# Kernel tuning notes

Hardware: AMD Instinct MI355X
Metric: run time of the kernel (lower is better)

The kernel has to match this reference:

```python
import jax, jax.numpy as jnp
import numpy as np

VOCAB = 128000
D = 256
N_BUBBLES = 256
N_EQ_STEPS = 5
SEQ_LEN = 512
ETA = 0.1      # relaxation rate toward input
KAPPA = 0.05   # mean-field coupling between bubbles


def setup_inputs() -> dict:
    key = jax.random.key(0)
    k1, k2, k3 = jax.random.split(key, 3)
    embed = jax.random.normal(k1, (VOCAB, D), dtype=jnp.float32)
    bubbles = jax.random.normal(k2, (N_BUBBLES, D), dtype=jnp.float32)
    memory_decay_base = jnp.asarray(0.8, dtype=jnp.float32)
    novelty_sensitivity = jnp.asarray(1.0, dtype=jnp.float32)
    tokens = jax.random.randint(k3, (SEQ_LEN,), 0, VOCAB, dtype=jnp.int64)
    return {"embed": embed, "bubbles": bubbles,
            "memory_decay_base": memory_decay_base,
            "novelty_sensitivity": novelty_sensitivity,
            "tokens": tokens}


def _foam_forward(x, bubbles):
    """x: [d]. Equilibrate bubble states, build density matrix, eigen-spectrum."""
    s = bubbles  # [n_bubbles, d]
    for _ in range(N_EQ_STEPS):  # fixed small hyperparam loop
        s = s + ETA * (x[None, :] - s) + KAPPA * (s.mean(axis=0, keepdims=True) - s)
        s = s / (jnp.linalg.norm(s, axis=-1, keepdims=True) + 1e-10)
    rho = (s.T @ s) / s.shape[0]  # [d, d] PSD, trace ~ 1
    w = jnp.linalg.eigvalsh(rho)  # ascending eigenvalues [d]
    w = jnp.clip(w, 0.0)
    output_dist = w / (w.sum() + 1e-10)
    return s, output_dist


def reference(embed, bubbles, memory_decay_base, novelty_sensitivity, tokens):
    sens = jnp.abs(novelty_sensitivity)

    def step(memory, tok):
        x = embed[tok]                      # [d]
        mem_mean = memory.mean(axis=0)      # [d]
        mem_norm = jnp.linalg.norm(mem_mean) + 1e-10
        x_norm = jnp.linalg.norm(x) + 1e-10
        novelty = jnp.where(mem_norm > 1e-8,
                            1.0 - jnp.dot(x, mem_mean) / (x_norm * mem_norm),
                            1.0)
        decay = jax.nn.sigmoid(memory_decay_base - sens * novelty)
        x_with_memory = x + decay * mem_mean
        eq, output_dist = _foam_forward(x_with_memory, bubbles)
        memory = decay * memory + (1.0 - decay) * eq
        return memory, output_dist

    memory0 = jnp.zeros_like(bubbles)  # [n_bubbles, d]
    _, dists = jax.lax.scan(step, memory0, tokens)
    return dists  # [seq_len, d] per-step eigenvalue distributions of rho
```

## Files before the change

### kernel.cpp

```cpp
#include <hip/hip_runtime.h>
#include <hip/hip_fp16.h>
#include <math.h>

#define SEQ 512
#define ETA 0.1f
#define KAPPA 0.05f
#define AA 0.85f

typedef _Float16 f16x8 __attribute__((ext_vector_type(8)));
typedef float f32x4 __attribute__((ext_vector_type(4)));

#define WS_G    ((size_t)0)
#define WS_GD   ((size_t)65536)
#define WS_M0   ((size_t)65792)
#define WS_BX   ((size_t)66048)
#define WS_X2   ((size_t)197120)
#define WS_ZS   ((size_t)197632)
#define WS_YS   ((size_t)328704)
#define WS_GS   ((size_t)459776)
#define WS_HS   ((size_t)984064)
#define WS_ALS  ((size_t)986112)
#define WS_BETS ((size_t)1117184)
#define WS_CT   ((size_t)1772544)

__device__ __forceinline__ float wred_sum(float v) {
#pragma unroll
  for (int m = 1; m < 64; m <<= 1) v += __shfl_xor(v, m, 64);
  return v;
}
__device__ __forceinline__ float wred_min(float v) {
#pragma unroll
  for (int m = 1; m < 64; m <<= 1) v = fminf(v, __shfl_xor(v, m, 64));
  return v;
}
__device__ __forceinline__ float wred_max(float v) {
#pragma unroll
  for (int m = 1; m < 64; m <<= 1) v = fmaxf(v, __shfl_xor(v, m, 64));
  return v;
}
__device__ __forceinline__ float rfl(float x) {
  return __builtin_bit_cast(float, __builtin_amdgcn_readfirstlane(__builtin_bit_cast(int, x)));
}

__global__ void k0_gram(const float* __restrict__ B, float* __restrict__ ws) {
  float* G = ws + WS_G;
  float* Gd = ws + WS_GD;
  __shared__ float bi[256];
  const int i = blockIdx.x, j = threadIdx.x;
  bi[j] = B[(size_t)i * 256 + j];
  __syncthreads();
  float a0 = 0.f, a1 = 0.f, a2 = 0.f, a3 = 0.f;
#pragma unroll
  for (int c = 0; c < 256; c += 4) {
    float4 b4 = *(const float4*)&B[(size_t)j * 256 + c];
    a0 = fmaf(bi[c + 0], b4.x, a0);
    a1 = fmaf(bi[c + 1], b4.y, a1);
    a2 = fmaf(bi[c + 2], b4.z, a2);
    a3 = fmaf(bi[c + 3], b4.w, a3);
  }
  float acc = (a0 + a1) + (a2 + a3);
  G[(size_t)i * 256 + j] = acc;
  if (i == j) Gd[i] = acc;
}

__global__ void k0_m0(const float* __restrict__ B, float* __restrict__ ws) {
  float* M0 = ws + WS_M0;
  const int d = threadIdx.x;
  float acc = 0.f;
  for (int i = 0; i < 256; ++i) acc += B[(size_t)i * 256 + d];
  M0[d] = acc * (1.0f / 256.0f);
}

__global__ void k0_bx(const float* __restrict__ B, const float* __restrict__ embed,
                      const int* __restrict__ toks, float* __restrict__ ws) {
  float* BX = ws + WS_BX;
  float* X2 = ws + WS_X2;
  __shared__ float xs[256];
  __shared__ float red[4];
  const int t = blockIdx.x, i = threadIdx.x;
  const int lane = i & 63, wid = i >> 6;
  const int tok = toks[t];
  float xv = embed[(size_t)tok * 256 + i];
  xs[i] = xv;
  float p = wred_sum(xv * xv);
  if (lane == 0) red[wid] = p;
  __syncthreads();
  if (i == 0) X2[t] = red[0] + red[1] + red[2] + red[3];
  float a0 = 0.f, a1 = 0.f, a2 = 0.f, a3 = 0.f;
#pragma unroll
  for (int c = 0; c < 256; c += 4) {
    float4 b4 = *(const float4*)&B[(size_t)i * 256 + c];
    a0 = fmaf(xs[c + 0], b4.x, a0);
    a1 = fmaf(xs[c + 1], b4.y, a1);
    a2 = fmaf(xs[c + 2], b4.z, a2);
    a3 = fmaf(xs[c + 3], b4.w, a3);
  }
  BX[(size_t)t * 256 + i] = (a0 + a1) + (a2 + a3);
}

__global__ __launch_bounds__(512, 1) void k1_seq(
    const float* __restrict__ embed, const int* __restrict__ toks,
    const float* __restrict__ mdbp, const float* __restrict__ sensp,
    float* __restrict__ ws) {
  const int tid = threadIdx.x;
  const int lane = tid & 63, wave = tid >> 6;
  const int i = tid >> 1, h = tid & 1;
  const float* G = ws + WS_G;
  const float* Gd = ws + WS_GD;
  const float* BX = ws + WS_BX;
  const float* X2 = ws + WS_X2;
  float* ZS = ws + WS_ZS;
  float* YS = ws + WS_YS;
  float* GS = ws + WS_GS;
  float* HS = ws + WS_HS;
  float* ALS = ws + WS_ALS;
  float* BETS = ws + WS_BETS;

  __shared__ __align__(16) float gcur[256];
  __shared__ __align__(16) float dp[6][256];
  __shared__ float dres_s[8];
  __shared__ float bbar_s[8];

  float Gq[128];
  {
    const float4* gr = (const float4*)(G + (size_t)i * 256 + (size_t)h * 128);
#pragma unroll
    for (int j4 = 0; j4 < 32; ++j4) {
      float4 v = gr[j4];
      Gq[4 * j4 + 0] = v.x; Gq[4 * j4 + 1] = v.y;
      Gq[4 * j4 + 2] = v.z; Gq[4 * j4 + 3] = v.w;
    }
  }
  const float Gdi = Gd[i];
  const float mdb = rfl(mdbp[0]);
  const float sens = fabsf(rfl(sensp[0]));

  float q0i;
  {
    float s = 0.f;
#pragma unroll
    for (int j = 0; j < 128; ++j) s += Gq[j];
    s += __shfl_xor(s, 1, 64);
    q0i = s * (1.0f / 256.0f);
  }
  float x_c = embed[(size_t)toks[0] * 256 + i];
  float bx_c = BX[i];
  float x2_c = rfl(X2[0]);
  if (h == 0) dp[0][i] = q0i; else dp[1][i] = bx_c;
  __syncthreads();
  if (wave < 2) {
    float4 v4 = ((const float4*)&dp[wave][0])[lane];
    float r_ = (v4.x + v4.y) + (v4.z + v4.w);
    r_ = wred_sum(r_);
    if (lane == 0) dres_s[wave] = r_ * (1.0f / 256.0f);
  }
  __syncthreads();
  const float c00 = rfl(dres_s[0]);
  float mbx_c = rfl(dres_s[1]);

  float Zi = 0.f, yi = 0.f, wi = 0.f;
  float mm2 = 0.f, mw = 0.f, dotxm = 0.f;

#pragma unroll 1
  for (int t = 0; t < SEQ; ++t) {
    const int tn = (t + 1 < SEQ) ? (t + 1) : t;
    const int tokn = toks[tn];
    const float x_n = embed[(size_t)tokn * 256 + i];
    const float bx_n = BX[(size_t)tn * 256 + i];
    const float x2_n = rfl(X2[tn]);

    const float memnorm = sqrtf(fmaxf(mm2, 0.f)) + 1e-10f;
    const float xnorm = sqrtf(x2_c) + 1e-10f;
    const float nov = (memnorm > 1e-8f) ? (1.0f - dotxm / (xnorm * memnorm)) : 1.0f;
    const float dec = 1.0f / (1.0f + expf(-(mdb - sens * nov)));
    const float od = 1.0f - dec;
    const float ri = bx_c + dec * wi;
    const float XM2 = x2_c + 2.f * dec * dotxm + dec * dec * mm2;
    const float mean_r = mbx_c + dec * mw;
    if (h == 0) ZS[(size_t)t * 256 + i] = dec * Zi;
    else        YS[(size_t)t * 256 + i] = x_c + dec * yi;

    float qhist[6], ghist[6], bmat[5], hls[6], xmm[5], bbar[5];
    float alpha;
    {
      qhist[0] = q0i; ghist[0] = 1.0f / 256.0f; hls[0] = 0.f;
      const float xmm0 = mean_r;
      const float tki = ETA * ri + KAPPA * q0i;
      const float CC00 = (ETA * ETA) * XM2 + 2.f * (ETA * KAPPA) * xmm0 +
                         (KAPPA * KAPPA) * c00;
      const float n2 = fmaxf(AA * AA * Gdi + 2.f * AA * tki + CC00, 0.f);
      const float inv = 1.0f / (sqrtf(n2) + 1e-10f);
      bmat[0] = inv; alpha = AA * inv; xmm[0] = xmm0;
      if (h == 0) dp[0][i] = inv;
    }
    __syncthreads();
    if (wave == 0) {
      float4 v4 = ((const float4*)&dp[0][0])[lane];
      float r_ = (v4.x + v4.y) + (v4.z + v4.w);
      r_ = wred_sum(r_);
      if (lane == 0) bbar_s[0] = r_ * (1.0f / 256.0f);
    }
    __syncthreads();
    bbar[0] = rfl(bbar_s[0]);

#pragma unroll
    for (int k = 1; k <= 5; ++k) {
      float hk = 0.f, gk = alpha * (1.0f / 256.0f);
#pragma unroll
      for (int l = 0; l < 5; ++l)
        if (l < k) {
          hk += bbar[l] * (ETA + KAPPA * hls[l]);
          gk += KAPPA * bbar[l] * ghist[l];
        }
      ghist[k] = gk; hls[k] = hk;
      if (k <= 4) {
        if (h == 0) GS[(size_t)(k - 1) * (SEQ * 256) + (size_t)t * 256 + i] = gk;
        if (tid == 0) HS[(size_t)(k - 1) * SEQ + t] = hk;
      }
      if (h == 0) gcur[i] = gk;
      __syncthreads();
      float a0 = 0.f, a1 = 0.f, a2 = 0.f, a3 = 0.f;
      const float4* gseg = (const float4*)&gcur[h * 128];
#pragma unroll
      for (int j4 = 0; j4 < 32; ++j4) {
        float4 g4 = gseg[j4];
        a0 = fmaf(Gq[4 * j4 + 0], g4.x, a0);
        a1 = fmaf(Gq[4 * j4 + 1], g4.y, a1);
        a2 = fmaf(Gq[4 * j4 + 2], g4.z, a2);
        a3 = fmaf(Gq[4 * j4 + 3], g4.w, a3);
      }
      float acc = (a0 + a1) + (a2 + a3);
      acc += __shfl_xor(acc, 1, 64);
      const float qk = acc + hk * ri;
      qhist[k] = qk;
      const int nv = (k < 5) ? (k + 2) : 4;
      if (k < 5) {
#pragma unroll
        for (int v = 0; v < 6; ++v)
          if ((v & 1) == h && v < nv)
            dp[v][i] = (v <= k) ? gk * qhist[v] : ri * gk;
      } else {
        if (h == 0) { dp[0][i] = gk * qk;  dp[2][i] = wi * gk; }
        else        { dp[1][i] = ri * gk;  dp[3][i] = qk * (1.0f / 256.0f); }
      }
      __syncthreads();
      if (wave < nv) {
        float4 v4 = ((const float4*)&dp[wave][0])[lane];
        float r_ = (v4.x + v4.y) + (v4.z + v4.w);
        r_ = wred_sum(r_);
        if (lane == 0) dres_s[wave] = r_;
      }
      __syncthreads();
      if (k < 5) {
        float dres[6];
#pragma unroll
        for (int v = 0; v < 6; ++v) if (v < nv) dres[v] = rfl(dres_s[v]);
        const float xmmk = dres[k + 1] + hk * XM2;
        const float tki = ETA * ri + KAPPA * qk;
        float sc = alpha * tki;
#pragma unroll
        for (int jj = 0; jj < 4; ++jj)
          if (jj < k) {
            const float MMjk = dres[jj] + hk * xmm[jj];
            const float CCjk = (ETA * ETA) * XM2 + (ETA * KAPPA) * (xmm[jj] + xmmk) +
                               (KAPPA * KAPPA) * MMjk;
            sc += bmat[jj] * CCjk;
          }
        const float MMkk = dres[k] + hk * xmmk;
        const float CCkk = (ETA * ETA) * XM2 + 2.f * (ETA * KAPPA) * xmmk +
                           (KAPPA * KAPPA) * MMkk;
        const float n2 = fmaxf(AA * AA + 2.f * AA * sc + CCkk, 0.f);
        const float inv = 1.0f / (sqrtf(n2) + 1e-10f);
#pragma unroll
        for (int jj = 0; jj < 4; ++jj) if (jj < k) bmat[jj] *= AA * inv;
        bmat[k] = inv; alpha *= AA * inv; xmm[k] = xmmk;
#pragma unroll
        for (int v = 0; v < 5; ++v)
          if ((v & 1) == h && v <= k) dp[v][i] = bmat[v];
        __syncthreads();
        if (wave <= k) {
          float4 v4 = ((const float4*)&dp[wave][0])[lane];
          float r_ = (v4.x + v4.y) + (v4.z + v4.w);
          r_ = wred_sum(r_);
          if (lane == 0) bbar_s[wave] = r_ * (1.0f / 256.0f);
        }
        __syncthreads();
#pragma unroll
        for (int l = 0; l < 5; ++l) if (l <= k) bbar[l] = rfl(bbar_s[l]);
      } else {
        const float A5 = rfl(dres_s[0]);
        const float B5 = rfl(dres_s[1]);
        const float C5 = rfl(dres_s[2]);
        const float mq5 = rfl(dres_s[3]);
        const float h5 = hk, g5 = gk, q5 = qk;
        const float xmm5 = B5 + h5 * XM2;
        const float m52 = A5 + h5 * xmm5;
        const float cmm5 = C5 + h5 * (dotxm + dec * mm2);
        const float lamc = dec * (1.0f + od * h5);
        Zi = lamc * Zi + od * g5;
        yi = lamc * yi + od * h5 * x_c;
        wi = dec * wi + od * q5;
        mm2 = fmaxf(dec * dec * mm2 + 2.f * dec * od * cmm5 + od * od * m52, 0.f);
        mw = dec * mw + od * mq5;
        if (h == 0) {
          ALS[(size_t)t * 256 + i] = alpha;
          BETS[(size_t)1 * (SEQ * 256) + (size_t)t * 256 + i] = bmat[1];
          BETS[(size_t)3 * (SEQ * 256) + (size_t)t * 256 + i] = bmat[3];
          dp[0][i] = bx_n * Zi + x_n * yi;
        } else {
          BETS[(size_t)0 * (SEQ * 256) + (size_t)t * 256 + i] = bmat[0];
          BETS[(size_t)2 * (SEQ * 256) + (size_t)t * 256 + i] = bmat[2];
          BETS[(size_t)4 * (SEQ * 256) + (size_t)t * 256 + i] = bmat[4];
          dp[1][i] = bx_n;
        }
        __syncthreads();
        if (wave < 2) {
          float4 v4 = ((const float4*)&dp[wave][0])[lane];
          float r_ = (v4.x + v4.y) + (v4.z + v4.w);
          r_ = wred_sum(r_);
          if (lane == 0) dres_s[4 + wave] = (wave == 0) ? r_ : r_ * (1.0f / 256.0f);
        }
        __syncthreads();
        dotxm = rfl(dres_s[4]);
        mbx_c = rfl(dres_s[5]);
      }
    }
    x_c = x_n; bx_c = bx_n; x2_c = x2_n;
  }
}

__global__ void k15_cvec(const float* __restrict__ B, float* __restrict__ ws) {
  const float* ZS = ws + WS_ZS;
  const float* YS = ws + WS_YS;
  const float* GS = ws + WS_GS;
  const float* HS = ws + WS_HS;
  const float* M0 = ws + WS_M0;
  float* CT = ws + WS_CT;
  const int t = blockIdx.x, d = threadIdx.x;
  __shared__ float zs[256], g1[256], g2[256], g3[256], g4[256];
  zs[d] = ZS[(size_t)t * 256 + d];
  g1[d] = GS[0 * (SEQ * 256) + (size_t)t * 256 + d];
  g2[d] = GS[1 * (SEQ * 256) + (size_t)t * 256 + d];
  g3[d] = GS[2 * (SEQ * 256) + (size_t)t * 256 + d];
  g4[d] = GS[3 * (SEQ * 256) + (size_t)t * 256 + d];
  __syncthreads();
  float xa = 0.f, b1 = 0.f, b2 = 0.f, b3 = 0.f, b4 = 0.f;
  for (int ii = 0; ii < 256; ++ii) {
    const float Bv = B[(size_t)ii * 256 + d];
    xa = fmaf(zs[ii], Bv, xa);
    b1 = fmaf(g1[ii], Bv, b1);
    b2 = fmaf(g2[ii], Bv, b2);
    b3 = fmaf(g3[ii], Bv, b3);
    b4 = fmaf(g4[ii], Bv, b4);
  }
  const float xm = YS[(size_t)t * 256 + d] + xa;
  float* ctt = CT + (size_t)t * 1280;
  ctt[0 * 256 + d] = ETA * xm + KAPPA * M0[d];
  const float h1 = HS[0 * SEQ + t], h2 = HS[1 * SEQ + t];
  const float h3 = HS[2 * SEQ + t], h4 = HS[3 * SEQ + t];
  ctt[1 * 256 + d] = (ETA + KAPPA * h1) * xm + KAPPA * b1;
  ctt[2 * 256 + d] = (ETA + KAPPA * h2) * xm + KAPPA * b2;
  ctt[3 * 256 + d] = (ETA + KAPPA * h3) * xm + KAPPA * b3;
  ctt[4 * 256 + d] = (ETA + KAPPA * h4) * xm + KAPPA * b4;
}

__global__ __launch_bounds__(1024, 4) void k2_eig(
    const float* __restrict__ B, const float* __restrict__ ws,
    float* __restrict__ out) {
  const int t = blockIdx.x;
  const int tid = threadIdx.x;
  const int lane = tid & 63, wid = tid >> 6;
  const float* CT = ws + WS_CT + (size_t)t * 1280;
  const float* ALS = ws + WS_ALS + (size_t)t * 256;
  const float* BETS = ws + WS_BETS;

  __shared__ __align__(16) unsigned char bigbuf[135168];
  _Float16* sT = (_Float16*)bigbuf;
  float* pk = (float*)bigbuf;
  __shared__ __align__(16) float ct[1280];
  __shared__ float vx[256], pv[256], qv[256];
  __shared__ float dd[256], ee[256], e2[256], lamv[256];
  __shared__ float red[16];

  for (int idx = tid; idx < 1280; idx += 1024) ct[idx] = CT[idx];
  __syncthreads();

  {
    const int r = tid >> 2, q = tid & 3;
    const float al = ALS[r];
    const float be0 = BETS[(size_t)0 * (SEQ * 256) + (size_t)t * 256 + r];
    const float be1 = BETS[(size_t)1 * (SEQ * 256) + (size_t)t * 256 + r];
    const float be2 = BETS[(size_t)2 * (SEQ * 256) + (size_t)t * 256 + r];
    const float be3 = BETS[(size_t)3 * (SEQ * 256) + (size_t)t * 256 + r];
    const float be4 = BETS[(size_t)4 * (SEQ * 256) + (size_t)t * 256 + r];
#pragma unroll
    for (int j4 = 0; j4 < 16; ++j4) {
      const int d0 = q * 64 + j4 * 4;
      const float4 Bv = *(const float4*)&B[(size_t)r * 256 + d0];
      const float4 c0 = *(const float4*)&ct[0 * 256 + d0];
      const float4 c1 = *(const float4*)&ct[1 * 256 + d0];
      const float4 c2 = *(const float4*)&ct[2 * 256 + d0];
      const float4 c3 = *(const float4*)&ct[3 * 256 + d0];
      const float4 c4 = *(const float4*)&ct[4 * 256 + d0];
      const float s0 = al * Bv.x + be0 * c0.x + be1 * c1.x + be2 * c2.x + be3 * c3.x + be4 * c4.x;
      const float s1 = al * Bv.y + be0 * c0.y + be1 * c1.y + be2 * c2.y + be3 * c3.y + be4 * c4.y;
      const float s2 = al * Bv.z + be0 * c0.z + be1 * c1.z + be2 * c2.z + be3 * c3.z + be4 * c4.z;
      const float s3 = al * Bv.w + be0 * c0.w + be1 * c1.w + be2 * c2.w + be3 * c3.w + be4 * c4.w;
      sT[(size_t)(d0 + 0) * 264 + r] = (_Float16)s0;
      sT[(size_t)(d0 + 1) * 264 + r] = (_Float16)s1;
      sT[(size_t)(d0 + 2) * 264 + r] = (_Float16)s2;
      sT[(size_t)(d0 + 3) * 264 + r] = (_Float16)s3;
    }
  }
  __syncthreads();

  f32x4 acc[4][4];
#pragma unroll
  for (int ti = 0; ti < 4; ++ti)
#pragma unroll
    for (int tj = 0; tj < 4; ++tj) {
      f32x4 z = {0.f, 0.f, 0.f, 0.f};
      acc[ti][tj] = z;
    }
  {
    const int Ib = (wid >> 2) * 4, Jb = (wid & 3) * 4;
    const int mr = lane & 15, kg = lane >> 4;
#pragma unroll 1
    for (int kb = 0; kb < 8; ++kb) {
      const int ko = kb * 32 + kg * 8;
      f16x8 aF[4], bF[4];
#pragma unroll
      for (int ti = 0; ti < 4; ++ti)
        aF[ti] = *(const f16x8*)&sT[(size_t)((Ib + ti) * 16 + mr) * 264 + ko];
#pragma unroll
      for (int tj = 0; tj < 4; ++tj)
        bF[tj] = *(const f16x8*)&sT[(size_t)((Jb + tj) * 16 + mr) * 264 + ko];
#pragma unroll
      for (int ti = 0; ti < 4; ++ti)
#pragma unroll
        for (int tj = 0; tj < 4; ++tj)
          acc[ti][tj] = __builtin_amdgcn_mfma_f32_16x16x32_f16(aF[ti], bF[tj], acc[ti][tj], 0, 0, 0);
    }
  }
  __syncthreads();
  {
    const int Ib = (wid >> 2) * 4, Jb = (wid & 3) * 4;
    const int cn = lane & 15, rg = lane >> 4;
#pragma unroll
    for (int ti = 0; ti < 4; ++ti)
#pragma unroll
      for (int tj = 0; tj < 4; ++tj) {
        const int C = (Jb + tj) * 16 + cn;
        const int Rb = (Ib + ti) * 16 + rg * 4;
#pragma unroll
        for (int rr = 0; rr < 4; ++rr) {
          const int R = Rb + rr;
          if (R >= C) pk[R * (R + 1) / 2 + C] = acc[ti][tj][rr] * (1.0f / 256.0f);
        }
      }
  }
  __syncthreads();

#pragma unroll 1
  for (int j = 0; j < 254; ++j) {
    const int m = 255 - j;
    const float x0 = pk[(j + 1) * (j + 2) / 2 + j];
    float ps = 0.f;
    if (tid < m) {
      const int gr = j + 1 + tid;
      const float xv_ = pk[gr * (gr + 1) / 2 + j];
      vx[tid] = xv_;
      ps = xv_ * xv_;
    }
    ps = wred_sum(ps);
    if (lane == 0) red[wid] = ps;
    __syncthreads();
    float sig2 = 0.f;
#pragma unroll
    for (int w = 0; w < 16; ++w) sig2 += red[w];
    const float sig = sqrtf(sig2);
    const float sg = (x0 >= 0.f) ? 1.f : -1.f;
    const bool live = (sig2 > 1e-26f);
    const float beta = live ? (1.0f / (sig * (sig + fabsf(x0)))) : 0.f;
    const float v0 = live ? (x0 + sg * sig) : 0.f;
    if (tid == 0) {
      dd[j] = pk[j * (j + 1) / 2 + j];
      ee[j] = live ? (-sg * sig) : x0;
      vx[0] = v0;
    }
    __syncthreads();
    {
      const int ri_ = tid >> 2, qd = tid & 3;
      float acc2 = 0.f;
      if (ri_ < m) {
        const int gr = j + 1 + ri_;
        const int c0 = (m * qd) >> 2, c1 = (m * (qd + 1)) >> 2;
        const int rowbase = gr * (gr + 1) / 2 + (j + 1);
        const int clend = min(c1, ri_ + 1);
        for (int c = c0; c < clend; ++c) acc2 = fmaf(pk[rowbase + c], vx[c], acc2);
        const int cu = max(c0, ri_ + 1);
        if (cu < c1) {
          int gc = j + 1 + cu;
          int ub = gc * (gc + 1) / 2 + gr;
          int stp = gc + 1;
          for (int c = cu; c < c1; ++c) { acc2 = fmaf(pk[ub], vx[c], acc2); ub += stp; ++stp; }
        }
      }
      acc2 += __shfl_xor(acc2, 1, 64);
      acc2 += __shfl_xor(acc2, 2, 64);
      float vpp = 0.f;
      if ((tid & 3) == 0 && (tid >> 2) < m) { pv[tid >> 2] = acc2; vpp = acc2 * vx[tid >> 2]; }
      vpp = wred_sum(vpp);
      if (lane == 0) red[wid] = vpp;
    }
    __syncthreads();
    float vtp = 0.f;
#pragma unroll
    for (int w = 0; w < 16; ++w) vtp += red[w];
    const float gamma = 0.5f * beta * beta * vtp;
    if (tid < m) qv[tid] = beta * pv[tid] - gamma * vx[tid];
    __syncthreads();
    {
      const int Q = tid >> 2, qd = tid & 3;
      const int i2 = m - 1 - Q;
      if (Q <= i2 && Q < m) {
        {
          const int gr = j + 1 + Q;
          const int rb = gr * (gr + 1) / 2 + (j + 1);
          const float vi = vx[Q], qi = qv[Q];
          const int cs = (qd * (Q + 1)) >> 2, ce = ((qd + 1) * (Q + 1)) >> 2;
          for (int c = cs; c < ce; ++c) pk[rb + c] -= vi * qv[c] + qi * vx[c];
        }
        if (i2 > Q) {
          const int gr = j + 1 + i2;
          const int rb = gr * (gr + 1) / 2 + (j + 1);
          const float vi = vx[i2], qi = qv[i2];
          const int cs = (qd * (i2 + 1)) >> 2, ce = ((qd + 1) * (i2 + 1)) >> 2;
          for (int c = cs; c < ce; ++c) pk[rb + c] -= vi * qv[c] + qi * vx[c];
        }
      }
    }
    __syncthreads();
  }
  if (tid == 0) {
    dd[254] = pk[254 * 255 / 2 + 254];
    dd[255] = pk[255 * 256 / 2 + 255];
    ee[254] = pk[255 * 256 / 2 + 254];
    ee[255] = 0.f;
  }
  __syncthreads();
  if (tid < 256) e2[tid] = ee[tid] * ee[tid];
  __syncthreads();
  float glo = 1e30f, ghi = -1e30f;
  if (tid < 256) {
    const float rad = fabsf(ee[tid]) + ((tid > 0) ? fabsf(ee[tid - 1]) : 0.f);
    glo = dd[tid] - rad;
    ghi = dd[tid] + rad;
  }
  {
    float v = wred_min(glo);
    if (lane == 0) red[wid] = v;
    __syncthreads();
    float lo0 = 1e30f;
#pragma unroll
    for (int w = 0; w < 16; ++w) lo0 = fminf(lo0, red[w]);
    __syncthreads();
    v = wred_max(ghi);
    if (lane == 0) red[wid] = v;
    __syncthreads();
    float hi0 = -1e30f;
#pragma unroll
    for (int w = 0; w < 16; ++w) hi0 = fmaxf(hi0, red[w]);
    lo0 -= 1e-3f + 1e-3f * fabsf(lo0);
    hi0 += 1e-3f + 1e-3f * fabsf(hi0);
    if (tid < 256) {
      float lo = lo0, hi = hi0;
      for (int it = 0; it < 21; ++it) {
        const float x = 0.5f * (lo + hi);
        int cnt = 0;
        float qq = dd[0] - x;
        cnt += (qq < 0.f);
        for (int ii = 1; ii < 256; ++ii) {
          float dn = qq;
          if (fabsf(dn) < 1e-25f) dn = (dn < 0.f) ? -1e-25f : 1e-25f;
          qq = (dd[ii] - x) - e2[ii - 1] * __builtin_amdgcn_rcpf(dn);
          cnt += (qq < 0.f);
        }
        if (cnt >= tid + 1) hi = x; else lo = x;
      }
      lamv[tid] = fmaxf(0.5f * (lo + hi), 0.f);
    }
  }
  __syncthreads();
  float sv = (tid < 256) ? lamv[tid] : 0.f;
  sv = wred_sum(sv);
  if (lane == 0) red[wid] = sv;
  __syncthreads();
  float S = 0.f;
#pragma unroll
  for (int w = 0; w < 16; ++w) S += red[w];
  if (tid < 256) out[(size_t)t * 256 + tid] = lamv[tid] / (S + 1e-10f);
}

extern "C" void kernel_launch(void* const* d_in, const int* in_sizes, int n_in,
                              void* d_out, int out_size, void* d_ws, size_t ws_size,
                              hipStream_t stream) {
  const float* embed = (const float*)d_in[0];
  const float* B = (const float*)d_in[1];
  const float* mdb = (const float*)d_in[2];
  const float* sens = (const float*)d_in[3];
  const int* toks = (const int*)d_in[4];
  float* out = (float*)d_out;
  float* ws = (float*)d_ws;

  k0_gram<<<dim3(256), dim3(256), 0, stream>>>(B, ws);
  k0_m0<<<dim3(1), dim3(256), 0, stream>>>(B, ws);
  k0_bx<<<dim3(SEQ), dim3(256), 0, stream>>>(B, embed, toks, ws);
  k1_seq<<<dim3(1), dim3(512), 0, stream>>>(embed, toks, mdb, sens, ws);
  k15_cvec<<<dim3(SEQ), dim3(256), 0, stream>>>(B, ws);
  k2_eig<<<dim3(SEQ), dim3(1024), 0, stream>>>(B, ws, out);
}
```

Baseline: 9.854 ms.

## Restructure sequential kernel to 1024 threads with fewer barriers per step

The single-block sequential recurrence kernel now uses 1024 threads, four per row instead of two, so each thread's register-resident Gram slice shrinks to 64 values. Shared-memory reduction passes with two barriers each are replaced by wave shuffles plus shared atomics into double-buffered accumulators, leaving about one barrier per inner step. Per-token setup is folded into the end of the previous step, and dot products against the Gram matrix are reconstructed algebraically from history so fewer reductions are needed. This targets barrier latency on the serial critical path, at the cost of atomic contention and changes to floating-point summation order.

```diff
diff --git a/kernel.cpp b/kernel.cpp
--- a/kernel.cpp
+++ b/kernel.cpp
@@ -98,13 +98,13 @@
   BX[(size_t)t * 256 + i] = (a0 + a1) + (a2 + a3);
 }
 
-__global__ __launch_bounds__(512, 1) void k1_seq(
+__global__ __launch_bounds__(1024, 1) void k1_seq(
     const float* __restrict__ embed, const int* __restrict__ toks,
     const float* __restrict__ mdbp, const float* __restrict__ sensp,
     float* __restrict__ ws) {
   const int tid = threadIdx.x;
-  const int lane = tid & 63, wave = tid >> 6;
-  const int i = tid >> 1, h = tid & 1;
+  const int lane = tid & 63;
+  const int i = tid >> 2, h = tid & 3;
   const float* G = ws + WS_G;
   const float* Gd = ws + WS_GD;
   const float* BX = ws + WS_BX;
@@ -116,20 +116,15 @@
   float* ALS = ws + WS_ALS;
   float* BETS = ws + WS_BETS;
 
-  __shared__ __align__(16) float gcur[256];
-  __shared__ __align__(16) float dp[6][256];
-  __shared__ float dres_s[8];
-  __shared__ float bbar_s[8];
-
-  float Gq[128];
-  {
-    const float4* gr = (const float4*)(G + (size_t)i * 256 + (size_t)h * 128);
-#pragma unroll
-    for (int j4 = 0; j4 < 32; ++j4) {
-      float4 v = gr[j4];
-      Gq[4 * j4 + 0] = v.x; Gq[4 * j4 + 1] = v.y;
-      Gq[4 * j4 + 2] = v.z; Gq[4 * j4 + 3] = v.w;
-    }
+  __shared__ __align__(16) float gcur[4 * 68];
+  __shared__ float dresb[2][8];
+  __shared__ float bbarb[2][8];
+
+  float4 Gq[16];
+  {
+    const float4* gp = (const float4*)(G + (size_t)i * 256 + (size_t)h * 64);
+#pragma unroll
+    for (int j = 0; j < 16; ++j) Gq[j] = gp[j];
   }
   const float Gdi = Gd[i];
   const float mdb = rfl(mdbp[0]);
@@ -139,27 +134,62 @@
   {
     float s = 0.f;
 #pragma unroll
-    for (int j = 0; j < 128; ++j) s += Gq[j];
+    for (int j = 0; j < 16; ++j) s += (Gq[j].x + Gq[j].y) + (Gq[j].z + Gq[j].w);
     s += __shfl_xor(s, 1, 64);
+    s += __shfl_xor(s, 2, 64);
     q0i = s * (1.0f / 256.0f);
   }
+
   float x_c = embed[(size_t)toks[0] * 256 + i];
   float bx_c = BX[i];
   float x2_c = rfl(X2[0]);
-  if (h == 0) dp[0][i] = q0i; else dp[1][i] = bx_c;
-  __syncthreads();
-  if (wave < 2) {
-    float4 v4 = ((const float4*)&dp[wave][0])[lane];
-    float r_ = (v4.x + v4.y) + (v4.z + v4.w);
-    r_ = wred_sum(r_);
-    if (lane == 0) dres_s[wave] = r_ * (1.0f / 256.0f);
-  }
-  __syncthreads();
-  const float c00 = rfl(dres_s[0]);
-  float mbx_c = rfl(dres_s[1]);
+
+  if (tid < 16) dresb[tid >> 3][tid & 7] = 0.f;
+  else if (tid < 32) bbarb[(tid - 16) >> 3][tid & 7] = 0.f;
+  __syncthreads();
+  {
+    float mv0 = 0.f;
+    if (h == 0) mv0 = q0i * (1.0f / 256.0f);
+    else if (h == 1) mv0 = bx_c * (1.0f / 256.0f);
+#pragma unroll
+    for (int m = 4; m <= 32; m <<= 1) mv0 += __shfl_xor(mv0, m, 64);
+    if (lane < 2) atomicAdd(&dresb[0][lane], mv0);
+  }
+  __syncthreads();
+  const float c00 = rfl(dresb[0][0]);
+  float mbx = rfl(dresb[0][1]);
 
   float Zi = 0.f, yi = 0.f, wi = 0.f;
   float mm2 = 0.f, mw = 0.f, dotxm = 0.f;
+
+  float dec = 1.0f / (1.0f + expf(-(mdb - sens)));
+  float od = 1.0f - dec;
+  float ri = bx_c;
+  float XM2 = x2_c;
+  float mean_r = mbx;
+  if (h == 0) ZS[i] = 0.f;
+  else if (h == 1) YS[i] = x_c;
+
+  float gh[6], Ggh[6], hhv[6], bmat[5], xmm[5], alpha;
+  gh[0] = 1.0f / 256.0f; Ggh[0] = q0i; hhv[0] = 0.f;
+  {
+    const float xmm0 = mean_r;
+    const float tki = ETA * ri + KAPPA * q0i;
+    const float CC00 = (ETA * ETA) * XM2 + 2.f * (ETA * KAPPA) * xmm0 +
+                       (KAPPA * KAPPA) * c00;
+    const float n2 = fmaxf(AA * AA * Gdi + 2.f * AA * tki + CC00, 0.f);
+    const float inv = 1.0f / (sqrtf(n2) + 1e-10f);
+    bmat[0] = inv; alpha = AA * inv; xmm[0] = xmm0;
+  }
+  if (h == 0) gcur[(i >> 6) * 68 + (i & 63)] = alpha;
+  {
+    float bv0 = (h == 0) ? bmat[0] : 0.f;
+#pragma unroll
+    for (int m = 4; m <= 32; m <<= 1) bv0 += __shfl_xor(bv0, m, 64);
+    if (lane == 0) atomicAdd(&bbarb[1][0], bv0);
+  }
+  __syncthreads();
+  int pq = 1;
 
 #pragma unroll 1
   for (int t = 0; t < SEQ; ++t) {
@@ -168,93 +198,75 @@
     const float x_n = embed[(size_t)tokn * 256 + i];
     const float bx_n = BX[(size_t)tn * 256 + i];
     const float x2_n = rfl(X2[tn]);
-
-    const float memnorm = sqrtf(fmaxf(mm2, 0.f)) + 1e-10f;
-    const float xnorm = sqrtf(x2_c) + 1e-10f;
-    const float nov = (memnorm > 1e-8f) ? (1.0f - dotxm / (xnorm * memnorm)) : 1.0f;
-    const float dec = 1.0f / (1.0f + expf(-(mdb - sens * nov)));
-    const float od = 1.0f - dec;
-    const float ri = bx_c + dec * wi;
-    const float XM2 = x2_c + 2.f * dec * dotxm + dec * dec * mm2;
-    const float mean_r = mbx_c + dec * mw;
-    if (h == 0) ZS[(size_t)t * 256 + i] = dec * Zi;
-    else        YS[(size_t)t * 256 + i] = x_c + dec * yi;
-
-    float qhist[6], ghist[6], bmat[5], hls[6], xmm[5], bbar[5];
-    float alpha;
-    {
-      qhist[0] = q0i; ghist[0] = 1.0f / 256.0f; hls[0] = 0.f;
-      const float xmm0 = mean_r;
-      const float tki = ETA * ri + KAPPA * q0i;
-      const float CC00 = (ETA * ETA) * XM2 + 2.f * (ETA * KAPPA) * xmm0 +
-                         (KAPPA * KAPPA) * c00;
-      const float n2 = fmaxf(AA * AA * Gdi + 2.f * AA * tki + CC00, 0.f);
-      const float inv = 1.0f / (sqrtf(n2) + 1e-10f);
-      bmat[0] = inv; alpha = AA * inv; xmm[0] = xmm0;
-      if (h == 0) dp[0][i] = inv;
-    }
-    __syncthreads();
-    if (wave == 0) {
-      float4 v4 = ((const float4*)&dp[0][0])[lane];
-      float r_ = (v4.x + v4.y) + (v4.z + v4.w);
-      r_ = wred_sum(r_);
-      if (lane == 0) bbar_s[0] = r_ * (1.0f / 256.0f);
-    }
-    __syncthreads();
-    bbar[0] = rfl(bbar_s[0]);
+    float q5sav = 0.f;
 
 #pragma unroll
     for (int k = 1; k <= 5; ++k) {
-      float hk = 0.f, gk = alpha * (1.0f / 256.0f);
+      if (tid < 8) dresb[1 - pq][tid] = 0.f;
+      else if (tid < 16) bbarb[1 - pq][tid - 8] = 0.f;
+      float4 av = {0.f, 0.f, 0.f, 0.f};
+      const float4* gc4 = (const float4*)&gcur[h * 68];
+#pragma unroll
+      for (int j = 0; j < 16; ++j) {
+        const float4 g4 = gc4[j];
+        av.x = fmaf(Gq[j].x, g4.x, av.x);
+        av.y = fmaf(Gq[j].y, g4.y, av.y);
+        av.z = fmaf(Gq[j].z, g4.z, av.z);
+        av.w = fmaf(Gq[j].w, g4.w, av.w);
+      }
+      float M = (av.x + av.y) + (av.z + av.w);
+      M += __shfl_xor(M, 1, 64);
+      M += __shfl_xor(M, 2, 64);
+      float hk = 0.f, gk = alpha * (1.0f / 256.0f), Ggk = M * (1.0f / 256.0f);
 #pragma unroll
       for (int l = 0; l < 5; ++l)
         if (l < k) {
-          hk += bbar[l] * (ETA + KAPPA * hls[l]);
-          gk += KAPPA * bbar[l] * ghist[l];
-        }
-      ghist[k] = gk; hls[k] = hk;
+          const float bb = rfl(bbarb[pq][l]) * (1.0f / 256.0f);
+          hk += bb * (ETA + KAPPA * hhv[l]);
+          gk = fmaf(KAPPA * bb, gh[l], gk);
+          Ggk = fmaf(KAPPA * bb, Ggh[l], Ggk);
+        }
+      const float qk = Ggk + hk * ri;
+      gh[k] = gk; Ggh[k] = Ggk; hhv[k] = hk;
       if (k <= 4) {
-        if (h == 0) GS[(size_t)(k - 1) * (SEQ * 256) + (size_t)t * 256 + i] = gk;
+        if (h == 2) GS[(size_t)(k - 1) * (SEQ * 256) + (size_t)t * 256 + i] = gk;
         if (tid == 0) HS[(size_t)(k - 1) * SEQ + t] = hk;
       }
-      if (h == 0) gcur[i] = gk;
+      float vv[8];
+      if (k < 5) {
+#pragma unroll
+        for (int l = 0; l < 8; ++l) {
+          if (l <= k) vv[l] = gk * (Ggh[l] + hhv[l] * ri);
+          else if (l == k + 1) vv[l] = ri * gk;
+          else vv[l] = 0.f;
+        }
+      } else {
+        q5sav = qk;
+        vv[0] = gk * qk;
+        vv[1] = ri * gk;
+        vv[2] = wi * gk;
+        vv[3] = qk * (1.0f / 256.0f);
+        vv[4] = bx_n * Zi + x_n * yi;
+        vv[5] = bx_n * gk;
+        vv[6] = x_n * x_c;
+        vv[7] = bx_n * (1.0f / 256.0f);
+      }
+      float mv0 = (h == 0) ? vv[0] : (h == 1) ? vv[1] : (h == 2) ? vv[2] : vv[3];
+      float mv1 = (h == 0) ? vv[4] : (h == 1) ? vv[5] : (h == 2) ? vv[6] : vv[7];
+#pragma unroll
+      for (int m = 4; m <= 32; m <<= 1) {
+        mv0 += __shfl_xor(mv0, m, 64);
+        mv1 += __shfl_xor(mv1, m, 64);
+      }
+      const int nv = (k < 5) ? (k + 2) : 8;
+      if (lane < 8 && lane < nv) atomicAdd(&dresb[pq][lane], lane < 4 ? mv0 : mv1);
       __syncthreads();
-      float a0 = 0.f, a1 = 0.f, a2 = 0.f, a3 = 0.f;
-      const float4* gseg = (const float4*)&gcur[h * 128];
-#pragma unroll
-      for (int j4 = 0; j4 < 32; ++j4) {
-        float4 g4 = gseg[j4];
-        a0 = fmaf(Gq[4 * j4 + 0], g4.x, a0);
-        a1 = fmaf(Gq[4 * j4 + 1], g4.y, a1);
-        a2 = fmaf(Gq[4 * j4 + 2], g4.z, a2);
-        a3 = fmaf(Gq[4 * j4 + 3], g4.w, a3);
-      }
-      float acc = (a0 + a1) + (a2 + a3);
-      acc += __shfl_xor(acc, 1, 64);
-      const float qk = acc + hk * ri;
-      qhist[k] = qk;
-      const int nv = (k < 5) ? (k + 2) : 4;
+
       if (k < 5) {
-#pragma unroll
-        for (int v = 0; v < 6; ++v)
-          if ((v & 1) == h && v < nv)
-            dp[v][i] = (v <= k) ? gk * qhist[v] : ri * gk;
-      } else {
-        if (h == 0) { dp[0][i] = gk * qk;  dp[2][i] = wi * gk; }
-        else        { dp[1][i] = ri * gk;  dp[3][i] = qk * (1.0f / 256.0f); }
-      }
-      __syncthreads();
-      if (wave < nv) {
-        float4 v4 = ((const float4*)&dp[wave][0])[lane];
-        float r_ = (v4.x + v4.y) + (v4.z + v4.w);
-        r_ = wred_sum(r_);
-        if (lane == 0) dres_s[wave] = r_;
-      }
-      __syncthreads();
-      if (k < 5) {
-        float dres[6];
-#pragma unroll
-        for (int v = 0; v < 6; ++v) if (v < nv) dres[v] = rfl(dres_s[v]);
+        float dres[7];
+#pragma unroll
+        for (int l = 0; l < 7; ++l)
+          if (l <= k + 1) dres[l] = rfl(dresb[pq][l]);
         const float xmmk = dres[k + 1] + hk * XM2;
         const float tki = ETA * ri + KAPPA * qk;
         float sc = alpha * tki;
@@ -264,7 +276,7 @@
             const float MMjk = dres[jj] + hk * xmm[jj];
             const float CCjk = (ETA * ETA) * XM2 + (ETA * KAPPA) * (xmm[jj] + xmmk) +
                                (KAPPA * KAPPA) * MMjk;
-            sc += bmat[jj] * CCjk;
+            sc = fmaf(bmat[jj], CCjk, sc);
           }
         const float MMkk = dres[k] + hk * xmmk;
         const float CCkk = (ETA * ETA) * XM2 + 2.f * (ETA * KAPPA) * xmmk +
@@ -272,60 +284,86 @@
         const float n2 = fmaxf(AA * AA + 2.f * AA * sc + CCkk, 0.f);
         const float inv = 1.0f / (sqrtf(n2) + 1e-10f);
 #pragma unroll
-        for (int jj = 0; jj < 4; ++jj) if (jj < k) bmat[jj] *= AA * inv;
-        bmat[k] = inv; alpha *= AA * inv; xmm[k] = xmmk;
-#pragma unroll
-        for (int v = 0; v < 5; ++v)
-          if ((v & 1) == h && v <= k) dp[v][i] = bmat[v];
+        for (int jj = 0; jj < 4; ++jj)
+          if (jj < k) bmat[jj] *= AA * inv;
+        bmat[k] = inv;
+        alpha *= AA * inv;
+        xmm[k] = xmmk;
+        if (k == 4) {
+          if (h == 3) ALS[(size_t)t * 256 + i] = alpha;
+          if (h == 0) {
+            BETS[(size_t)0 * (SEQ * 256) + (size_t)t * 256 + i] = bmat[0];
+            BETS[(size_t)4 * (SEQ * 256) + (size_t)t * 256 + i] = bmat[4];
+          } else if (h == 1) {
+            BETS[(size_t)1 * (SEQ * 256) + (size_t)t * 256 + i] = bmat[1];
+          } else if (h == 2) {
+            BETS[(size_t)2 * (SEQ * 256) + (size_t)t * 256 + i] = bmat[2];
+          } else {
+            BETS[(size_t)3 * (SEQ * 256) + (size_t)t * 256 + i] = bmat[3];
+          }
+        }
+        if (h == 0) gcur[(i >> 6) * 68 + (i & 63)] = alpha;
+        float bv0 = (h == 0) ? bmat[0]
+                  : (h == 1) ? ((k >= 1) ? bmat[1] : 0.f)
+                  : (h == 2) ? ((k >= 2) ? bmat[2] : 0.f)
+                             : ((k >= 3) ? bmat[3] : 0.f);
+        float bv1 = (h == 0 && k >= 4) ? bmat[4] : 0.f;
+#pragma unroll
+        for (int m = 4; m <= 32; m <<= 1) {
+          bv0 += __shfl_xor(bv0, m, 64);
+          bv1 += __shfl_xor(bv1, m, 64);
+        }
+        if (lane < 8 && lane <= k)
+          atomicAdd(&bbarb[1 - pq][lane], lane < 4 ? bv0 : bv1);
         __syncthreads();
-        if (wave <= k) {
-          float4 v4 = ((const float4*)&dp[wave][0])[lane];
-          float r_ = (v4.x + v4.y) + (v4.z + v4.w);
-          r_ = wred_sum(r_);
-          if (lane == 0) bbar_s[wave] = r_ * (1.0f / 256.0f);
-        }
-        __syncthreads();
-#pragma unroll
-        for (int l = 0; l < 5; ++l) if (l <= k) bbar[l] = rfl(bbar_s[l]);
+        pq ^= 1;
       } else {
-        const float A5 = rfl(dres_s[0]);
-        const float B5 = rfl(dres_s[1]);
-        const float C5 = rfl(dres_s[2]);
-        const float mq5 = rfl(dres_s[3]);
-        const float h5 = hk, g5 = gk, q5 = qk;
-        const float xmm5 = B5 + h5 * XM2;
-        const float m52 = A5 + h5 * xmm5;
-        const float cmm5 = C5 + h5 * (dotxm + dec * mm2);
+        float dr[8];
+#pragma unroll
+        for (int l = 0; l < 8; ++l) dr[l] = rfl(dresb[pq][l]);
+        const float h5 = hhv[5];
+        const float g5 = gh[5];
+        const float q5 = q5sav;
+        const float xmm5 = dr[1] + h5 * XM2;
+        const float m52 = dr[0] + h5 * xmm5;
+        const float cmm5 = dr[2] + h5 * (dotxm + dec * mm2);
         const float lamc = dec * (1.0f + od * h5);
         Zi = lamc * Zi + od * g5;
         yi = lamc * yi + od * h5 * x_c;
         wi = dec * wi + od * q5;
         mm2 = fmaxf(dec * dec * mm2 + 2.f * dec * od * cmm5 + od * od * m52, 0.f);
-        mw = dec * mw + od * mq5;
-        if (h == 0) {
-          ALS[(size_t)t * 256 + i] = alpha;
-          BETS[(size_t)1 * (SEQ * 256) + (size_t)t * 256 + i] = bmat[1];
-          BETS[(size_t)3 * (SEQ * 256) + (size_t)t * 256 + i] = bmat[3];
-          dp[0][i] = bx_n * Zi + x_n * yi;
-        } else {
-          BETS[(size_t)0 * (SEQ * 256) + (size_t)t * 256 + i] = bmat[0];
-          BETS[(size_t)2 * (SEQ * 256) + (size_t)t * 256 + i] = bmat[2];
-          BETS[(size_t)4 * (SEQ * 256) + (size_t)t * 256 + i] = bmat[4];
-          dp[1][i] = bx_n;
-        }
+        mw = dec * mw + od * dr[3];
+        dotxm = lamc * dr[4] + od * (dr[5] + h5 * dr[6]);
+        mbx = dr[7];
+        x_c = x_n; bx_c = bx_n; x2_c = x2_n;
+        const float memnorm = sqrtf(mm2) + 1e-10f;
+        const float xnorm = sqrtf(x2_c) + 1e-10f;
+        const float nov = (memnorm > 1e-8f) ? (1.0f - dotxm / (xnorm * memnorm)) : 1.0f;
+        dec = 1.0f / (1.0f + expf(-(mdb - sens * nov)));
+        od = 1.0f - dec;
+        ri = bx_c + dec * wi;
+        XM2 = x2_c + 2.f * dec * dotxm + dec * dec * mm2;
+        mean_r = mbx + dec * mw;
+        if (t + 1 < SEQ) {
+          if (h == 0) ZS[(size_t)(t + 1) * 256 + i] = dec * Zi;
+          else if (h == 1) YS[(size_t)(t + 1) * 256 + i] = x_c + dec * yi;
+        }
+        const float xmm0 = mean_r;
+        const float tki = ETA * ri + KAPPA * q0i;
+        const float CC00 = (ETA * ETA) * XM2 + 2.f * (ETA * KAPPA) * xmm0 +
+                           (KAPPA * KAPPA) * c00;
+        const float n2 = fmaxf(AA * AA * Gdi + 2.f * AA * tki + CC00, 0.f);
+        const float inv = 1.0f / (sqrtf(n2) + 1e-10f);
+        bmat[0] = inv; alpha = AA * inv; xmm[0] = xmm0;
+        if (h == 0) gcur[(i >> 6) * 68 + (i & 63)] = alpha;
+        float bv0 = (h == 0) ? bmat[0] : 0.f;
+#pragma unroll
+        for (int m = 4; m <= 32; m <<= 1) bv0 += __shfl_xor(bv0, m, 64);
+        if (lane == 0) atomicAdd(&bbarb[1 - pq][0], bv0);
         __syncthreads();
-        if (wave < 2) {
-          float4 v4 = ((const float4*)&dp[wave][0])[lane];
-          float r_ = (v4.x + v4.y) + (v4.z + v4.w);
-          r_ = wred_sum(r_);
-          if (lane == 0) dres_s[4 + wave] = (wave == 0) ? r_ : r_ * (1.0f / 256.0f);
-        }
-        __syncthreads();
-        dotxm = rfl(dres_s[4]);
-        mbx_c = rfl(dres_s[5]);
-      }
-    }
-    x_c = x_n; bx_c = bx_n; x2_c = x2_n;
+        pq ^= 1;
+      }
+    }
   }
 }
 
@@ -616,7 +654,7 @@
   k0_gram<<<dim3(256), dim3(256), 0, stream>>>(B, ws);
   k0_m0<<<dim3(1), dim3(256), 0, stream>>>(B, ws);
   k0_bx<<<dim3(SEQ), dim3(256), 0, stream>>>(B, embed, toks, ws);
-  k1_seq<<<dim3(1), dim3(512), 0, stream>>>(embed, toks, mdb, sens, ws);
+  k1_seq<<<dim3(1), dim3(1024), 0, stream>>>(embed, toks, mdb, sens, ws);
   k15_cvec<<<dim3(SEQ), dim3(256), 0, stream>>>(B, ws);
   k2_eig<<<dim3(SEQ), dim3(1024), 0, stream>>>(B, ws, out);
 }
```

New measurement: 12.01 ms. +21.8%, slower.
